# Optimization experiments

Measured on AMD Instinct MI355X. Metric: run time of the kernel, lower is better.

Reference implementation:

```python
import jax, jax.numpy as jnp
import numpy as np

T = 2048      # total tokens (single prefill sequence)
HID = 2048    # hidden_size
H = 16        # num k-heads == num v-heads
DK = 128      # key head dim
DV = 128      # value head dim
K = 4         # causal conv kernel width
EPS = 1e-6


def setup_inputs() -> dict:
    key = jax.random.key(0)
    ks = jax.random.split(key, 10)
    n = lambda k, shape, sc: (jax.random.normal(k, shape, jnp.float32) * sc)
    return {
        "hidden_states": n(ks[0], (T, HID), 1.0),
        "Wq": n(ks[1], (HID, H * DK), 0.02),
        "Wk": n(ks[2], (HID, H * DK), 0.02),
        "Wv": n(ks[3], (HID, H * DV), 0.02),
        "Wb": n(ks[4], (HID, H), 0.02),
        "conv_wq": n(ks[5], (H * DK, K), 0.5),
        "conv_wk": n(ks[6], (H * DK, K), 0.5),
        "conv_wv": n(ks[7], (H * DV, K), 0.5),
        "o_norm_w": jnp.ones((DV,), jnp.float32),
        "Wo": n(ks[8], (HID, HID), 0.02),
    }


def _causal_conv_silu(x, w):
    # x: [T, D], w: [D, K] depthwise causal conv, then SiLU (matches causal_conv1d_fn)
    xp = jnp.pad(x, ((K - 1, 0), (0, 0)))
    y = sum(xp[j:j + T] * w[:, j] for j in range(K))
    return jax.nn.silu(y)


def _l2norm(x):
    return x * jax.lax.rsqrt(jnp.sum(x * x, axis=-1, keepdims=True) + EPS)


def reference(hidden_states, Wq, Wk, Wv, Wb, conv_wq, conv_wk, conv_wv, o_norm_w, Wo):
    # projections [T, H*D]
    q = _causal_conv_silu(hidden_states @ Wq, conv_wq).reshape(T, H, DK)
    k = _causal_conv_silu(hidden_states @ Wk, conv_wk).reshape(T, H, DK)
    v = _causal_conv_silu(hidden_states @ Wv, conv_wv).reshape(T, H, DV)
    beta = jax.nn.sigmoid(hidden_states @ Wb)  # [T, H]

    # qk l2-norm + scale (FLA chunk_delta_rule defaults)
    q = _l2norm(q) * (DK ** -0.5)
    k = _l2norm(k)

    # delta-rule recurrence: S <- S + beta * k (v - k^T S)
    def step(S, inp):
        q_t, k_t, v_t, b_t = inp            # [H,DK],[H,DK],[H,DV],[H]
        kS = jnp.einsum('hk,hkv->hv', k_t, S)
        delta = b_t[:, None] * (v_t - kS)   # [H, DV]
        S = S + jnp.einsum('hk,hv->hkv', k_t, delta)
        o_t = jnp.einsum('hk,hkv->hv', q_t, S)
        return S, o_t

    S0 = jnp.zeros((H, DK, DV), jnp.float32)
    _, o = jax.lax.scan(step, S0, (q, k, v, beta))  # o: [T, H, DV]

    # per-head RMSNorm on value head dim
    o = o * jax.lax.rsqrt(jnp.mean(o * o, axis=-1, keepdims=True) + EPS) * o_norm_w
    out = o.reshape(T, H * DV) @ Wo
    return out
```

## Files before the change

kernel.cpp:

```cpp
#include <hip/hip_runtime.h>

typedef unsigned short u16;
typedef __attribute__((ext_vector_type(4))) unsigned short u16x4;
typedef __attribute__((ext_vector_type(8))) unsigned short u16x8;
typedef __attribute__((ext_vector_type(8))) short short8;
typedef __attribute__((ext_vector_type(4))) float f32x4;

#define DEVI __device__ __forceinline__

DEVI u16 f2b(float f) {
  union { float f; unsigned u; } x; x.f = f;
  unsigned r = (x.u + 0x7fffu + ((x.u >> 16) & 1u)) >> 16;
  return (u16)r;
}
DEVI float b2f(u16 h) {
  union { unsigned u; float f; } x; x.u = ((unsigned)h) << 16;
  return x.f;
}
DEVI f32x4 mfma_bf16(short8 a, short8 b, f32x4 c) {
  return __builtin_amdgcn_mfma_f32_16x16x32_bf16(a, b, c, 0, 0, 0);
}
DEVI void gl2lds16(const u16* g, u16* l) {
  __builtin_amdgcn_global_load_lds((__attribute__((address_space(1))) void*)g,
                                   (__attribute__((address_space(3))) void*)l,
                                   16, 0, 0);
}
DEVI void barrier_lds() {
  asm volatile("s_waitcnt lgkmcnt(0)\n\ts_barrier" ::: "memory");
}

__global__ void k_cvt(const float* __restrict__ src, u16* __restrict__ dst, int n4,
                      const float* __restrict__ Wb, u16* __restrict__ WbT) {
  int b = blockIdx.x;
  if (b < 4096) {
    int i = b * 256 + threadIdx.x;
    if (i < n4) {
      float4 v = ((const float4*)src)[i];
      u16x4 r; r.x = f2b(v.x); r.y = f2b(v.y); r.z = f2b(v.z); r.w = f2b(v.w);
      ((u16x4*)dst)[i] = r;
    }
  } else {
    int j = (b - 4096) * 256 + threadIdx.x;
    int n = j >> 11, k = j & 2047;
    WbT[j] = f2b(Wb[k * 16 + n]);
  }
}

__global__ __launch_bounds__(256)
void k_transpose4(const float* __restrict__ s0, const float* __restrict__ s1,
                  const float* __restrict__ s2, const float* __restrict__ s3,
                  u16* __restrict__ d0, u16* __restrict__ d1,
                  u16* __restrict__ d2, u16* __restrict__ d3) {
  const int RC = 2048;
  const float* src = (blockIdx.z == 0) ? s0 : (blockIdx.z == 1) ? s1 : (blockIdx.z == 2) ? s2 : s3;
  u16* dst = (blockIdx.z == 0) ? d0 : (blockIdx.z == 1) ? d1 : (blockIdx.z == 2) ? d2 : d3;
  __shared__ u16 tile[64 * 66];
  int bx = blockIdx.x << 6, by = blockIdx.y << 6;
  int x = threadIdx.x & 63, g = threadIdx.x >> 6;
#pragma unroll
  for (int i = 0; i < 16; ++i) {
    int r = (i << 2) + g;
    tile[x * 66 + r] = f2b(src[(size_t)(by + r) * RC + bx + x]);
  }
  __syncthreads();
#pragma unroll
  for (int i = 0; i < 16; ++i) {
    int r = (i << 2) + g;
    dst[(size_t)(bx + r) * RC + by + x] = tile[r * 66 + x];
  }
}

__global__ __launch_bounds__(256, 2)
void k_gemm_bt(const u16* __restrict__ A, const u16* __restrict__ BT,
               float* __restrict__ Cf, u16* __restrict__ Cb,
               int M, int N, int K, int outbf) {
  __shared__ __align__(16) u16 As[4096];
  __shared__ __align__(16) u16 Bs[4096];
  const int tid = threadIdx.x, wave = tid >> 6, lane = tid & 63;
  const long bm = (long)blockIdx.y << 7, bn = (long)blockIdx.x << 7;
  const int r0 = (wave << 4) + (lane >> 2);
  const int kof = (((lane & 3) ^ ((lane >> 3) & 3)) << 3);
  const u16* gA = A + (bm + r0) * (long)K + kof;
  const u16* gB = BT + (bn + r0) * (long)K + kof;
  u16* lA = As + (wave << 9);
  u16* lB = Bs + (wave << 9);
  const long stepR = (long)64 * K;
  const int wr = (wave >> 1) << 6, wc = (wave & 1) << 6;
  const int fr = lane & 15, fq = (lane >> 4) << 3;
  const int sw = ((fr >> 1) & 3) << 3;
  const int fqs = fq ^ sw;
  f32x4 acc[4][4];
#pragma unroll
  for (int i = 0; i < 4; ++i)
#pragma unroll
    for (int j = 0; j < 4; ++j) acc[i][j] = (f32x4){0.f, 0.f, 0.f, 0.f};
  for (int k0 = 0; k0 < K; k0 += 32) {
    gl2lds16(gA + k0, lA);
    gl2lds16(gA + stepR + k0, lA + 2048);
    gl2lds16(gB + k0, lB);
    gl2lds16(gB + stepR + k0, lB + 2048);
    __syncthreads();
    short8 af[4], bfr[4];
#pragma unroll
    for (int t = 0; t < 4; ++t)
      af[t] = *(const short8*)&As[(wr + (t << 4) + fr) * 32 + fqs];
#pragma unroll
    for (int t = 0; t < 4; ++t)
      bfr[t] = *(const short8*)&Bs[(wc + (t << 4) + fr) * 32 + fqs];
#pragma unroll
    for (int i = 0; i < 4; ++i)
#pragma unroll
      for (int j = 0; j < 4; ++j)
        acc[i][j] = mfma_bf16(af[i], bfr[j], acc[i][j]);
    __syncthreads();
  }
  const int er = (lane >> 4) << 2, ec = lane & 15;
#pragma unroll
  for (int i = 0; i < 4; ++i)
#pragma unroll
    for (int j = 0; j < 4; ++j)
#pragma unroll
      for (int r = 0; r < 4; ++r) {
        long row = bm + wr + (i << 4) + er + r;
        long col = bn + wc + (j << 4) + ec;
        if (outbf) Cb[row * N + col] = f2b(acc[i][j][r]);
        else       Cf[row * N + col] = acc[i][j][r];
      }
}

__global__ __launch_bounds__(256, 4)
void k_beta(const u16* __restrict__ Xb, const u16* __restrict__ WbT,
            float* __restrict__ beta) {
  __shared__ float part[4][256];
  int tid = threadIdx.x, w = tid >> 6, lane = tid & 63;
  int t0 = blockIdx.x << 4;
  int fr = lane & 15, fq = (lane >> 4) << 3;
  const u16* ap = Xb + (size_t)(t0 + fr) * 2048 + (w << 9) + fq;
  const u16* bp = WbT + (size_t)fr * 2048 + (w << 9) + fq;
  f32x4 acc = {0.f, 0.f, 0.f, 0.f};
#pragma unroll
  for (int ks = 0; ks < 16; ++ks)
    acc = mfma_bf16(*(const short8*)(ap + (ks << 5)), *(const short8*)(bp + (ks << 5)), acc);
  int er = (lane >> 4) << 2;
#pragma unroll
  for (int r = 0; r < 4; ++r) part[w][(er + r) * 16 + fr] = acc[r];
  __syncthreads();
  float s = part[0][tid] + part[1][tid] + part[2][tid] + part[3][tid];
  beta[(t0 << 4) + tid] = 1.f / (1.f + __expf(-s));
}

__global__ void k_conv(const u16* __restrict__ qkv,
                       const float* __restrict__ cwq, const float* __restrict__ cwk,
                       const float* __restrict__ cwv,
                       u16* __restrict__ qn, u16* __restrict__ kn, u16* __restrict__ vn) {
  int t = blockIdx.x, s = blockIdx.y;
  int kind = s >> 4, h = s & 15, d = threadIdx.x;
  int col = kind * 2048 + (h << 7) + d;
  const float* cw = (kind == 0) ? cwq : ((kind == 1) ? cwk : cwv);
  float4 w = *(const float4*)(cw + (size_t)((h << 7) + d) * 4);
  float x[4];
#pragma unroll
  for (int j = 0; j < 4; ++j) {
    int tt = t - 3 + j;
    x[j] = (tt >= 0) ? b2f(qkv[(size_t)tt * 6144 + col]) : 0.f;
  }
  float y = x[0] * w.x + x[1] * w.y + x[2] * w.z + x[3] * w.w;
  y = y / (1.f + __expf(-y));
  float sc = 1.f;
  __shared__ float red[2];
  if (kind < 2) {
    float ss = y * y;
#pragma unroll
    for (int off = 32; off; off >>= 1) ss += __shfl_down(ss, off, 64);
    int lane = threadIdx.x & 63, wv = threadIdx.x >> 6;
    if (lane == 0) red[wv] = ss;
    __syncthreads();
    float tot = red[0] + red[1];
    sc = rsqrtf(tot + 1e-6f);
    if (kind == 0) sc *= 0.08838834764831843f;
  }
  u16* dst = (kind == 0) ? qn : ((kind == 1) ? kn : vn);
  dst[((size_t)h << 18) + ((size_t)t << 7) + d] = f2b(y * sc);
}

__global__ __launch_bounds__(256, 2)
void k_prep(const u16* __restrict__ qn, const u16* __restrict__ kn, const u16* __restrict__ vn,
            const float* __restrict__ beta,
            u16* __restrict__ Gg, u16* __restrict__ Wg,
            u16* __restrict__ KTg, u16* __restrict__ UTg) {
  __shared__ __align__(16) char sm[70912];
  u16*  Kc  = (u16*)sm;
  u16*  Qc  = (u16*)(sm + 17408);
  u16*  Vc  = (u16*)(sm + 34816);
  u16*  KTl = (u16*)(sm + 52224);
  float* AL = (float*)(sm + 52224);
  float* Bl = (float*)(sm + 70656);
  u16*  WR  = Qc;
  int h = blockIdx.x, c = blockIdx.y;
  int tid = threadIdx.x, wave = tid >> 6, lane = tid & 63;
  size_t ch = (size_t)(c * 16 + h);
  const u16* kb = kn + ((size_t)h << 18) + ((size_t)c << 13);
  const u16* qb = qn + ((size_t)h << 18) + ((size_t)c << 13);
  const u16* vb = vn + ((size_t)h << 18) + ((size_t)c << 13);
#pragma unroll
  for (int s = 0; s < 4; ++s) {
    int e = (tid + (s << 8)) << 3;
    int t = e >> 7, d = e & 127;
    *(u16x8*)&Kc[t * 136 + d] = *(const u16x8*)(kb + e);
    *(u16x8*)&Qc[t * 136 + d] = *(const u16x8*)(qb + e);
    *(u16x8*)&Vc[t * 136 + d] = *(const u16x8*)(vb + e);
  }
  if (tid < 64) Bl[tid] = beta[((c << 6) + tid) * 16 + h];
  __syncthreads();
  int fr = lane & 15, fq = (lane >> 4) << 3, q4 = (lane >> 4) << 2;
  int arow = (wave << 4) + fr;
  f32x4 kk[4], qk[4];
#pragma unroll
  for (int ct = 0; ct < 4; ++ct) { kk[ct] = (f32x4){0.f,0.f,0.f,0.f}; qk[ct] = (f32x4){0.f,0.f,0.f,0.f}; }
#pragma unroll
  for (int ks = 0; ks < 4; ++ks) {
    short8 aK = *(const short8*)&Kc[arow * 136 + (ks << 5) + fq];
    short8 aQ = *(const short8*)&Qc[arow * 136 + (ks << 5) + fq];
#pragma unroll
    for (int ct = 0; ct < 4; ++ct) {
      short8 bK = *(const short8*)&Kc[((ct << 4) + fr) * 136 + (ks << 5) + fq];
      kk[ct] = mfma_bf16(aK, bK, kk[ct]);
      qk[ct] = mfma_bf16(aQ, bK, qk[ct]);
    }
  }
#pragma unroll
  for (int ct = 0; ct < 4; ++ct)
#pragma unroll
    for (int r = 0; r < 4; ++r) {
      int i = (wave << 4) + q4 + r, j = (ct << 4) + fr;
      Gg[(ch << 12) + i * 64 + j] = f2b((j <= i) ? qk[ct][r] : 0.f);
    }
  {
    int d = tid & 127, tg = tid >> 7;
#pragma unroll
    for (int it = 0; it < 4; ++it) {
      int t0 = (tg + (it << 1)) << 3;
      u16x8 pk;
#pragma unroll
      for (int j = 0; j < 8; ++j) pk[j] = Kc[(t0 + j) * 136 + d];
      *(u16x8*)&KTl[d * 72 + t0] = pk;
    }
  }
  __syncthreads();
#pragma unroll
  for (int it = 0; it < 4; ++it) {
    int idx = tid + (it << 8);
    int row = idx >> 3, j8 = (idx & 7) << 3;
    *(u16x8*)(KTg + (ch << 13) + (row << 6) + j8) = *(const u16x8*)&KTl[row * 72 + j8];
  }
  __syncthreads();
  {
    float bi[4];
#pragma unroll
    for (int r = 0; r < 4; ++r) bi[r] = Bl[(wave << 4) + q4 + r];
#pragma unroll
    for (int ct = 0; ct < 4; ++ct)
#pragma unroll
      for (int r = 0; r < 4; ++r) {
        int i = (wave << 4) + q4 + r, j = (ct << 4) + fr;
        AL[i * 64 + j] = (j < i) ? bi[r] * kk[ct][r] : 0.f;
      }
  }
  __syncthreads();
  float X[64];
  {
    const u16* colp = (tid < 128) ? (Kc + tid) : (Vc + (tid - 128));
#pragma unroll
    for (int t = 0; t < 64; ++t) X[t] = Bl[t] * b2f(colp[t * 136]);
#pragma unroll
    for (int r = 1; r < 64; ++r) {
      float s = 0.f;
      const float* Ar = &AL[r * 64];
      int r4 = r & ~3;
#pragma unroll
      for (int l = 0; l < 64; l += 4)
        if (l + 4 <= r) {
          float4 a = *(const float4*)(Ar + l);
          s += a.x * X[l] + a.y * X[l + 1] + a.z * X[l + 2] + a.w * X[l + 3];
        }
#pragma unroll
      for (int l = 0; l < 4; ++l)
        if (r4 + l < r) s += Ar[r4 + l] * X[r4 + l];
      X[r] -= s;
    }
  }
  __syncthreads();
  if (tid < 128) {
#pragma unroll
    for (int t = 0; t < 64; ++t) WR[t * 136 + tid] = f2b(X[t]);
  } else {
    int v = tid - 128;
    u16* dstr = UTg + (ch << 13) + (v << 6);
#pragma unroll
    for (int j = 0; j < 8; ++j) {
      u16x8 p;
#pragma unroll
      for (int e = 0; e < 8; ++e) p[e] = f2b(X[(j << 3) + e]);
      *(u16x8*)(dstr + (j << 3)) = p;
    }
  }
  __syncthreads();
#pragma unroll
  for (int it = 0; it < 4; ++it) {
    int idx = tid + (it << 8);
    int row = idx >> 4, j8 = (idx & 15) << 3;
    *(u16x8*)(Wg + (ch << 13) + (row << 7) + j8) = *(const u16x8*)&WR[row * 136 + j8];
  }
}

struct Frags { short8 q[4], w[4], g[2], k[4]; u16x4 u; };

DEVI void load_frags(Frags& f, const u16* qh, const u16* Wg, const u16* Gg,
                     const u16* KTg, const u16* UTg, int c, int h,
                     int trow, int fr, int fq, int q4, int w, int vbase) {
  const u16* qb = qh + ((size_t)((c << 6) + trow + fr) << 7) + fq;
#pragma unroll
  for (int ks = 0; ks < 4; ++ks) f.q[ks] = *(const short8*)(qb + (ks << 5));
  size_t ch = (size_t)(c * 16 + h);
  const u16* wb = Wg + (ch << 13) + ((size_t)(trow + fr) << 7) + fq;
#pragma unroll
  for (int ks = 0; ks < 4; ++ks) f.w[ks] = *(const short8*)(wb + (ks << 5));
  const u16* gb = Gg + (ch << 12) + ((size_t)(trow + fr) << 6) + fq;
#pragma unroll
  for (int ks = 0; ks < 2; ++ks) f.g[ks] = *(const short8*)(gb + (ks << 5));
  const u16* kbp = KTg + (ch << 13) + ((size_t)(w << 5) << 6) + fq;
#pragma unroll
  for (int dt = 0; dt < 2; ++dt)
#pragma unroll
    for (int ks = 0; ks < 2; ++ks)
      f.k[(dt << 1) | ks] = *(const short8*)(kbp + ((size_t)((dt << 4) + fr) << 6) + (ks << 5));
  f.u = *(const u16x4*)(UTg + (ch << 13) + ((size_t)(vbase + fr) << 6) + trow + q4);
}

DEVI void chunk_body(int c, Frags& f, u16* ST, u16* DT, float* oh,
                     int trow, int fr, int fq, int q4, int w, int vbase,
                     f32x4& S0, f32x4& S1) {
#pragma unroll
  for (int r = 0; r < 4; ++r) {
    ST[(q4 + r) * 136 + (w << 5) + fr] = f2b(S0[r]);
    ST[(q4 + r) * 136 + (w << 5) + 16 + fr] = f2b(S1[r]);
  }
  barrier_lds();
  short8 sf[4];
#pragma unroll
  for (int ks = 0; ks < 4; ++ks) sf[ks] = *(const short8*)&ST[fr * 136 + (ks << 5) + fq];
  f32x4 racc = {0.f,0.f,0.f,0.f}, oacc = {0.f,0.f,0.f,0.f};
#pragma unroll
  for (int ks = 0; ks < 4; ++ks) {
    racc = mfma_bf16(f.w[ks], sf[ks], racc);
    oacc = mfma_bf16(f.q[ks], sf[ks], oacc);
  }
#pragma unroll
  for (int r = 0; r < 4; ++r)
    DT[fr * 72 + trow + q4 + r] = f2b(b2f(f.u[r]) - racc[r]);
  barrier_lds();
  short8 df[2];
#pragma unroll
  for (int ks = 0; ks < 2; ++ks) df[ks] = *(const short8*)&DT[fr * 72 + (ks << 5) + fq];
#pragma unroll
  for (int ks = 0; ks < 2; ++ks) {
    oacc = mfma_bf16(f.g[ks], df[ks], oacc);
    S0 = mfma_bf16(df[ks], f.k[ks], S0);
    S1 = mfma_bf16(df[ks], f.k[2 | ks], S1);
  }
#pragma unroll
  for (int r = 0; r < 4; ++r)
    oh[(size_t)((c << 6) + trow + q4 + r) * 128 + vbase + fr] = oacc[r];
}

__global__ __launch_bounds__(256, 1)
void k_delta(const u16* __restrict__ qn, const u16* __restrict__ Wg,
             const u16* __restrict__ Gg, const u16* __restrict__ KTg,
             const u16* __restrict__ UTg, float* __restrict__ o) {
  __shared__ __align__(16) u16 ST[16 * 136];
  __shared__ __align__(16) u16 DT[16 * 72];
  int bx = blockIdx.x;
  int h = bx & 15, vbase = (bx >> 4) << 4;
  int tid = threadIdx.x, w = tid >> 6, lane = tid & 63;
  int fr = lane & 15, fq = (lane >> 4) << 3, q4 = (lane >> 4) << 2;
  int trow = w << 4;
  const u16* qh = qn + ((size_t)h << 18);
  float* oh = o + ((size_t)h << 18);
  f32x4 S0 = {0.f,0.f,0.f,0.f}, S1 = {0.f,0.f,0.f,0.f};
  Frags fa, fb;
  load_frags(fa, qh, Wg, Gg, KTg, UTg, 0, h, trow, fr, fq, q4, w, vbase);
  for (int c = 0; c < 32; c += 2) {
    int c1 = c + 1, c2 = (c + 2 < 32) ? c + 2 : 31;
    load_frags(fb, qh, Wg, Gg, KTg, UTg, c1, h, trow, fr, fq, q4, w, vbase);
    chunk_body(c, fa, ST, DT, oh, trow, fr, fq, q4, w, vbase, S0, S1);
    load_frags(fa, qh, Wg, Gg, KTg, UTg, c2, h, trow, fr, fq, q4, w, vbase);
    chunk_body(c1, fb, ST, DT, oh, trow, fr, fq, q4, w, vbase, S0, S1);
  }
}

__global__ void k_onorm(const float* __restrict__ o, const float* __restrict__ onw,
                        u16* __restrict__ onb) {
  int t = blockIdx.x, h = blockIdx.y, d = threadIdx.x;
  float x = o[((size_t)h << 18) + ((size_t)t << 7) + d];
  float ss = x * x;
#pragma unroll
  for (int off = 32; off; off >>= 1) ss += __shfl_down(ss, off, 64);
  __shared__ float red[2];
  int lane = d & 63, wv = d >> 6;
  if (lane == 0) red[wv] = ss;
  __syncthreads();
  float tot = red[0] + red[1];
  float y = x * rsqrtf(tot * (1.f / 128.f) + 1e-6f) * onw[d];
  onb[((size_t)t << 11) + (h << 7) + d] = f2b(y);
}

extern "C" void kernel_launch(void* const* d_in, const int* in_sizes, int n_in,
                              void* d_out, int out_size, void* d_ws, size_t ws_size,
                              hipStream_t stream) {
  (void)in_sizes; (void)n_in; (void)out_size; (void)ws_size;
  const float* hs  = (const float*)d_in[0];
  const float* Wq  = (const float*)d_in[1];
  const float* Wk  = (const float*)d_in[2];
  const float* Wv  = (const float*)d_in[3];
  const float* Wb  = (const float*)d_in[4];
  const float* cwq = (const float*)d_in[5];
  const float* cwk = (const float*)d_in[6];
  const float* cwv = (const float*)d_in[7];
  const float* onw = (const float*)d_in[8];
  const float* Wo  = (const float*)d_in[9];
  float* out = (float*)d_out;
  char* ws = (char*)d_ws;
  const size_t MB = 1ull << 20;
  u16*  Xb   = (u16*)(ws);
  u16*  WT   = (u16*)(ws + 8  * MB);
  u16*  WoT  = (u16*)(ws + 32 * MB);
  u16*  QKV  = (u16*)(ws + 40 * MB);
  u16*  Wg   = (u16*)(ws + 40 * MB);
  u16*  KTg  = (u16*)(ws + 48 * MB);
  u16*  UTg  = (u16*)(ws + 56 * MB);
  u16*  qn_  = (u16*)(ws + 64 * MB);
  u16*  kn_  = (u16*)(ws + 72 * MB);
  u16*  vn_  = (u16*)(ws + 80 * MB);
  float* beta= (float*)(ws + 88 * MB);
  u16*  WbT  = (u16*)(ws + 88 * MB + 512 * 1024);
  u16*  Gm   = (u16*)(ws + 89 * MB);
  float* o_  = (float*)(ws + 93 * MB);
  u16*  onb  = (u16*)(ws + 109 * MB);

  k_cvt<<<4224, 256, 0, stream>>>(hs, Xb, 2048 * 2048 / 4, Wb, WbT);
  k_transpose4<<<dim3(32, 32, 4), 256, 0, stream>>>(
      Wq, Wk, Wv, Wo, WT, WT + 2048 * 2048, WT + 2 * 2048 * 2048, WoT);
  k_gemm_bt<<<dim3(48, 16), 256, 0, stream>>>(Xb, WT, nullptr, QKV, 2048, 6144, 2048, 1);
  k_beta<<<128, 256, 0, stream>>>(Xb, WbT, beta);
  k_conv<<<dim3(2048, 48), 128, 0, stream>>>(QKV, cwq, cwk, cwv, qn_, kn_, vn_);
  k_prep<<<dim3(16, 32), 256, 0, stream>>>(qn_, kn_, vn_, beta, Gm, Wg, KTg, UTg);
  k_delta<<<128, 256, 0, stream>>>(qn_, Wg, Gm, KTg, UTg, o_);
  k_onorm<<<dim3(2048, 16), 128, 0, stream>>>(o_, onw, onb);
  k_gemm_bt<<<dim3(16, 16), 256, 0, stream>>>(onb, WoT, out, nullptr, 2048, 2048, 2048, 0);
}
```

Measured before the change: 388.8 us.

## Use 64-row tiles for output GEMM, bf16 delta output, raise occupancy

Adds a 64x128-tile GEMM variant for the final Wo projection, doubling the grid from 256 to 512 blocks so more CUs are busy on a 2048x2048 output. The delta kernel now writes its output in bf16 instead of fp32, halving the write traffic and the read traffic in the RMSNorm kernel. It also raises the launch-bounds occupancy hint on the main GEMM from 2 to 4 blocks per CU. The bf16 intermediate adds rounding before the norm, and the occupancy hint may force register limits or spills.

```diff
diff --git a/kernel.cpp b/kernel.cpp
--- a/kernel.cpp
+++ b/kernel.cpp
@@ -70,7 +70,7 @@
   }
 }
 
-__global__ __launch_bounds__(256, 2)
+__global__ __launch_bounds__(256, 4)
 void k_gemm_bt(const u16* __restrict__ A, const u16* __restrict__ BT,
                float* __restrict__ Cf, u16* __restrict__ Cb,
                int M, int N, int K, int outbf) {
@@ -87,8 +87,7 @@
   const long stepR = (long)64 * K;
   const int wr = (wave >> 1) << 6, wc = (wave & 1) << 6;
   const int fr = lane & 15, fq = (lane >> 4) << 3;
-  const int sw = ((fr >> 1) & 3) << 3;
-  const int fqs = fq ^ sw;
+  const int fqs = fq ^ (((fr >> 1) & 3) << 3);
   f32x4 acc[4][4];
 #pragma unroll
   for (int i = 0; i < 4; ++i)
@@ -125,6 +124,60 @@
         long col = bn + wc + (j << 4) + ec;
         if (outbf) Cb[row * N + col] = f2b(acc[i][j][r]);
         else       Cf[row * N + col] = acc[i][j][r];
+      }
+}
+
+__global__ __launch_bounds__(256, 4)
+void k_gemm_bt64(const u16* __restrict__ A, const u16* __restrict__ BT,
+                 float* __restrict__ Cf, int M, int N, int K) {
+  __shared__ __align__(16) u16 As[2048];
+  __shared__ __align__(16) u16 Bs[4096];
+  const int tid = threadIdx.x, wave = tid >> 6, lane = tid & 63;
+  const long bm = (long)blockIdx.y << 6, bn = (long)blockIdx.x << 7;
+  const int r0 = (wave << 4) + (lane >> 2);
+  const int kof = (((lane & 3) ^ ((lane >> 3) & 3)) << 3);
+  const u16* gA = A + (bm + r0) * (long)K + kof;
+  const u16* gB = BT + (bn + r0) * (long)K + kof;
+  u16* lA = As + (wave << 9);
+  u16* lB = Bs + (wave << 9);
+  const long stepR = (long)64 * K;
+  const int wr = (wave >> 1) << 5, wc = (wave & 1) << 6;
+  const int fr = lane & 15, fq = (lane >> 4) << 3;
+  const int fqs = fq ^ (((fr >> 1) & 3) << 3);
+  f32x4 acc[2][4];
+#pragma unroll
+  for (int i = 0; i < 2; ++i)
+#pragma unroll
+    for (int j = 0; j < 4; ++j) acc[i][j] = (f32x4){0.f, 0.f, 0.f, 0.f};
+  for (int k0 = 0; k0 < K; k0 += 32) {
+    gl2lds16(gA + k0, lA);
+    gl2lds16(gB + k0, lB);
+    gl2lds16(gB + stepR + k0, lB + 2048);
+    __syncthreads();
+    short8 af[2], bfr[4];
+#pragma unroll
+    for (int t = 0; t < 2; ++t)
+      af[t] = *(const short8*)&As[(wr + (t << 4) + fr) * 32 + fqs];
+#pragma unroll
+    for (int t = 0; t < 4; ++t)
+      bfr[t] = *(const short8*)&Bs[(wc + (t << 4) + fr) * 32 + fqs];
+#pragma unroll
+    for (int i = 0; i < 2; ++i)
+#pragma unroll
+      for (int j = 0; j < 4; ++j)
+        acc[i][j] = mfma_bf16(af[i], bfr[j], acc[i][j]);
+    __syncthreads();
+  }
+  const int er = (lane >> 4) << 2, ec = lane & 15;
+#pragma unroll
+  for (int i = 0; i < 2; ++i)
+#pragma unroll
+    for (int j = 0; j < 4; ++j)
+#pragma unroll
+      for (int r = 0; r < 4; ++r) {
+        long row = bm + wr + (i << 4) + er + r;
+        long col = bn + wc + (j << 4) + ec;
+        Cf[row * N + col] = acc[i][j][r];
       }
 }
 
@@ -337,7 +390,7 @@
   f.u = *(const u16x4*)(UTg + (ch << 13) + ((size_t)(vbase + fr) << 6) + trow + q4);
 }
 
-DEVI void chunk_body(int c, Frags& f, u16* ST, u16* DT, float* oh,
+DEVI void chunk_body(int c, Frags& f, u16* ST, u16* DT, u16* oh,
                      int trow, int fr, int fq, int q4, int w, int vbase,
                      f32x4& S0, f32x4& S1) {
 #pragma unroll
@@ -370,13 +423,13 @@
   }
 #pragma unroll
   for (int r = 0; r < 4; ++r)
-    oh[(size_t)((c << 6) + trow + q4 + r) * 128 + vbase + fr] = oacc[r];
+    oh[(size_t)((c << 6) + trow + q4 + r) * 128 + vbase + fr] = f2b(oacc[r]);
 }
 
 __global__ __launch_bounds__(256, 1)
 void k_delta(const u16* __restrict__ qn, const u16* __restrict__ Wg,
              const u16* __restrict__ Gg, const u16* __restrict__ KTg,
-             const u16* __restrict__ UTg, float* __restrict__ o) {
+             const u16* __restrict__ UTg, u16* __restrict__ o) {
   __shared__ __align__(16) u16 ST[16 * 136];
   __shared__ __align__(16) u16 DT[16 * 72];
   int bx = blockIdx.x;
@@ -385,7 +438,7 @@
   int fr = lane & 15, fq = (lane >> 4) << 3, q4 = (lane >> 4) << 2;
   int trow = w << 4;
   const u16* qh = qn + ((size_t)h << 18);
-  float* oh = o + ((size_t)h << 18);
+  u16* oh = o + ((size_t)h << 18);
   f32x4 S0 = {0.f,0.f,0.f,0.f}, S1 = {0.f,0.f,0.f,0.f};
   Frags fa, fb;
   load_frags(fa, qh, Wg, Gg, KTg, UTg, 0, h, trow, fr, fq, q4, w, vbase);
@@ -398,10 +451,10 @@
   }
 }
 
-__global__ void k_onorm(const float* __restrict__ o, const float* __restrict__ onw,
+__global__ void k_onorm(const u16* __restrict__ o, const float* __restrict__ onw,
                         u16* __restrict__ onb) {
   int t = blockIdx.x, h = blockIdx.y, d = threadIdx.x;
-  float x = o[((size_t)h << 18) + ((size_t)t << 7) + d];
+  float x = b2f(o[((size_t)h << 18) + ((size_t)t << 7) + d]);
   float ss = x * x;
 #pragma unroll
   for (int off = 32; off; off >>= 1) ss += __shfl_down(ss, off, 64);
@@ -444,7 +497,7 @@
   float* beta= (float*)(ws + 88 * MB);
   u16*  WbT  = (u16*)(ws + 88 * MB + 512 * 1024);
   u16*  Gm   = (u16*)(ws + 89 * MB);
-  float* o_  = (float*)(ws + 93 * MB);
+  u16*  o_   = (u16*)(ws + 93 * MB);
   u16*  onb  = (u16*)(ws + 109 * MB);
 
   k_cvt<<<4224, 256, 0, stream>>>(hs, Xb, 2048 * 2048 / 4, Wb, WbT);
@@ -456,5 +509,5 @@
   k_prep<<<dim3(16, 32), 256, 0, stream>>>(qn_, kn_, vn_, beta, Gm, Wg, KTg, UTg);
   k_delta<<<128, 256, 0, stream>>>(qn_, Wg, Gm, KTg, UTg, o_);
   k_onorm<<<dim3(2048, 16), 128, 0, stream>>>(o_, onw, onb);
-  k_gemm_bt<<<dim3(16, 16), 256, 0, stream>>>(onb, WoT, out, nullptr, 2048, 2048, 2048, 0);
-}
+  k_gemm_bt64<<<dim3(16, 32), 256, 0, stream>>>(onb, WoT, out, 2048, 2048, 2048);
+}
```

Result: faster. 374.5 us (-3.7%).
